# Kernel tuning notes

Hardware: AMD Instinct MI355X
Metric: run time of the kernel (lower is better)

The kernel has to match this reference:

```python
import jax, jax.numpy as jnp
import numpy as np

N = 2048          # num_nodes
F = 32            # out_features
B = 8             # batch size
DEG = 32          # avg degree for random adjacency


def _make_edge_mask(key):
    # adjacency with density DEG/N, diagonal forced to 1, plus leading ones column
    p = DEG / N
    adj = jax.random.bernoulli(key, p, (N, N))
    adj = adj | jnp.eye(N, dtype=bool)
    adj = jnp.concatenate([jnp.ones((N, 1), dtype=bool), adj], axis=1)  # [N, N+1]
    return ~adj  # True => masked (zeroed), matching mask = 1 - adj


def setup_inputs() -> dict:
    key = jax.random.key(0)
    k1, k2, k3, k4 = jax.random.split(key, 4)
    x = jax.random.normal(k1, (B, N + 1, N), dtype=jnp.float32)
    weight = jax.random.normal(k2, (N, N + 1, F), dtype=jnp.float32) * (1.0 / np.sqrt(N + 1))
    bias = jax.random.normal(k3, (F, N), dtype=jnp.float32) * 0.02
    edge_mask = _make_edge_mask(k4)  # [N, N+1] bool, True = zero
    return {"x": x, "weight": weight, "bias": bias, "edge_mask": edge_mask}


def reference(x, weight, bias, edge_mask):
    # x: [B, N+1, N] -> per-node rows [B, N, N+1]
    xt = jnp.transpose(x, (0, 2, 1))                       # [B, N, N+1]
    xm = jnp.where(edge_mask[None, :, :], 0.0, xt)          # masked_fill_
    # per-node matmul against its own weight slab [N+1, F]
    ans = jnp.einsum('bnk,nkf->bnf', xm, weight)            # [B, N, F]
    ans = jnp.transpose(ans, (0, 2, 1))                     # [B, F, N]
    return ans + bias[None, :, :]
```

## Files before the change

kernel.cpp:

```cpp
#include <hip/hip_runtime.h>


constexpr int N_ = 2048;
constexpr int K_ = 2049;
constexpr int F_ = 32;
constexpr int B_ = 8;
constexpr int CH = 9;
constexpr int CAPK = 192;

__global__ __launch_bounds__(256, 8) void snl_sparse2(
    const float* __restrict__ x,
    const float* __restrict__ w,
    const float* __restrict__ bias,
    const int*   __restrict__ em,
    float* __restrict__ out)
{
    const int bid = blockIdx.x;
    const int n   = ((bid & 7) << 8) | (bid >> 3);
    const int t   = threadIdx.x;
    const int lane   = t & 63;
    const int wid    = t >> 6;
    const int kphase = t >> 5;
    const int f      = t & 31;

    __shared__ int   s_cnt[CH * 4];
    __shared__ int   s_idx[CAPK];
    __shared__ float s_x[CAPK][B_];
    __shared__ float s_red[8][B_][F_];

    const int*   emn = em + (size_t)n * K_;
    const float* wn  = w  + (size_t)n * K_ * F_;

    int emr[CH];
    #pragma unroll
    for (int c = 0; c < CH - 1; ++c) emr[c] = emn[c * 256 + t];
    emr[CH - 1] = (t == 0) ? emn[2048] : 1;

    const unsigned long long lowmask = (1ull << lane) - 1ull;
    int woff[CH];
    unsigned actmask = 0;
    #pragma unroll
    for (int c = 0; c < CH; ++c) {
        const unsigned long long bal = __ballot(emr[c] == 0);
        if (lane == 0) s_cnt[c * 4 + wid] = __popcll(bal);
        woff[c] = __popcll(bal & lowmask);
        actmask |= (emr[c] == 0 ? 1u : 0u) << c;
    }
    __syncthreads();

    int ct = 0;
    #pragma unroll
    for (int c = 0; c < CH; ++c) {
        const int c0 = s_cnt[c * 4 + 0];
        const int c1 = s_cnt[c * 4 + 1];
        const int c2 = s_cnt[c * 4 + 2];
        const int c3 = s_cnt[c * 4 + 3];
        const int base = ct + ((wid > 0) ? c0 : 0) + ((wid > 1) ? c1 : 0) + ((wid > 2) ? c2 : 0);
        ct += c0 + c1 + c2 + c3;
        if ((actmask >> c) & 1u) {
            const int pos = base + woff[c];
            const int k   = c * 256 + t;
            if (pos < CAPK) {
                s_idx[pos] = k;
                const float* xp = x + (size_t)k * N_ + n;
                const float xv0 = xp[0 * (size_t)K_ * N_];
                const float xv1 = xp[1 * (size_t)K_ * N_];
                const float xv2 = xp[2 * (size_t)K_ * N_];
                const float xv3 = xp[3 * (size_t)K_ * N_];
                const float xv4 = xp[4 * (size_t)K_ * N_];
                const float xv5 = xp[5 * (size_t)K_ * N_];
                const float xv6 = xp[6 * (size_t)K_ * N_];
                const float xv7 = xp[7 * (size_t)K_ * N_];
                *reinterpret_cast<float4*>(&s_x[pos][0]) = make_float4(xv0, xv1, xv2, xv3);
                *reinterpret_cast<float4*>(&s_x[pos][4]) = make_float4(xv4, xv5, xv6, xv7);
            }
        }
    }

    const int ctc = (ct < CAPK) ? ct : CAPK;
    const int ctp = (ctc + 7) & ~7;
    if (t < ctp - ctc) {
        s_idx[ctc + t] = 0;
        *reinterpret_cast<float4*>(&s_x[ctc + t][0]) = make_float4(0.f, 0.f, 0.f, 0.f);
        *reinterpret_cast<float4*>(&s_x[ctc + t][4]) = make_float4(0.f, 0.f, 0.f, 0.f);
    }
    __syncthreads();

    const int tc = ctp >> 3;
    float acc[B_];
    #pragma unroll
    for (int b = 0; b < B_; ++b) acc[b] = 0.f;

    float wr[8];
    #pragma unroll
    for (int i = 0; i < 8; ++i) {
        if (i < tc) {
            const int j = kphase + i * 8;
            wr[i] = wn[(size_t)s_idx[j] * F_ + f];
        }
    }
    #pragma unroll
    for (int i = 0; i < 8; ++i) {
        if (i < tc) {
            const int j = kphase + i * 8;
            const float4 x0 = *reinterpret_cast<const float4*>(&s_x[j][0]);
            const float4 x1 = *reinterpret_cast<const float4*>(&s_x[j][4]);
            const float wv = wr[i];
            acc[0] = fmaf(x0.x, wv, acc[0]);
            acc[1] = fmaf(x0.y, wv, acc[1]);
            acc[2] = fmaf(x0.z, wv, acc[2]);
            acc[3] = fmaf(x0.w, wv, acc[3]);
            acc[4] = fmaf(x1.x, wv, acc[4]);
            acc[5] = fmaf(x1.y, wv, acc[5]);
            acc[6] = fmaf(x1.z, wv, acc[6]);
            acc[7] = fmaf(x1.w, wv, acc[7]);
        }
    }
    for (int j = kphase + 64; j < ctp; j += 8) {
        const float wv = wn[(size_t)s_idx[j] * F_ + f];
        const float4 x0 = *reinterpret_cast<const float4*>(&s_x[j][0]);
        const float4 x1 = *reinterpret_cast<const float4*>(&s_x[j][4]);
        acc[0] = fmaf(x0.x, wv, acc[0]);
        acc[1] = fmaf(x0.y, wv, acc[1]);
        acc[2] = fmaf(x0.z, wv, acc[2]);
        acc[3] = fmaf(x0.w, wv, acc[3]);
        acc[4] = fmaf(x1.x, wv, acc[4]);
        acc[5] = fmaf(x1.y, wv, acc[5]);
        acc[6] = fmaf(x1.z, wv, acc[6]);
        acc[7] = fmaf(x1.w, wv, acc[7]);
    }

    #pragma unroll
    for (int b = 0; b < B_; ++b) s_red[kphase][b][f] = acc[b];
    __syncthreads();

    {
        const int b  = t >> 5;
        const int ff = t & 31;
        float s = 0.f;
        #pragma unroll
        for (int p = 0; p < 8; ++p) s += s_red[p][b][ff];
        out[((size_t)b * F_ + ff) * N_ + n] = s + bias[(size_t)ff * N_ + n];
    }
}

extern "C" void kernel_launch(void* const* d_in, const int* in_sizes, int n_in,
                              void* d_out, int out_size, void* d_ws, size_t ws_size,
                              hipStream_t stream) {
    const float* x    = (const float*)d_in[0];
    const float* w    = (const float*)d_in[1];
    const float* bias = (const float*)d_in[2];
    const int*   em   = (const int*)d_in[3];
    float*       out  = (float*)d_out;

    snl_sparse2<<<dim3(N_), dim3(256), 0, stream>>>(x, w, bias, em, out);
}
```

Before: 21.04 us.

## Compact active indices per wavefront to drop block-wide barriers

Each wavefront now compacts its own active k indices into a private shared-memory list, so the block-wide prefix sum and two __syncthreads are no longer needed before the compute phase. The x gather is restructured so that 8 lanes load the 8 batch values of a slot in parallel, instead of one thread issuing 8 strided loads. Each wave then accumulates only its own slots with two k-phases, and the existing 8-way shared reduction combines the partial sums. A per-wave cap of 48 entries could drop nonzeros if one wave's 576 columns have more than 48 active entries, and load balance across waves depends on how the nonzeros are spread.

```diff
diff --git a/kernel.cpp b/kernel.cpp
--- a/kernel.cpp
+++ b/kernel.cpp
@@ -6,26 +6,23 @@
 constexpr int F_ = 32;
 constexpr int B_ = 8;
 constexpr int CH = 9;
-constexpr int CAPK = 192;
+constexpr int WCAP = 48;
 
-__global__ __launch_bounds__(256, 8) void snl_sparse2(
+__global__ __launch_bounds__(256, 8) void snl_sparse3(
     const float* __restrict__ x,
     const float* __restrict__ w,
     const float* __restrict__ bias,
     const int*   __restrict__ em,
     float* __restrict__ out)
 {
-    const int bid = blockIdx.x;
-    const int n   = ((bid & 7) << 8) | (bid >> 3);
-    const int t   = threadIdx.x;
-    const int lane   = t & 63;
-    const int wid    = t >> 6;
-    const int kphase = t >> 5;
-    const int f      = t & 31;
+    const int bid  = blockIdx.x;
+    const int n    = ((bid & 7) << 8) | (bid >> 3);
+    const int t    = threadIdx.x;
+    const int lane = t & 63;
+    const int wid  = t >> 6;
 
-    __shared__ int   s_cnt[CH * 4];
-    __shared__ int   s_idx[CAPK];
-    __shared__ float s_x[CAPK][B_];
+    __shared__ int   s_idx[4][WCAP];
+    __shared__ float s_x[4][WCAP][B_];
     __shared__ float s_red[8][B_][F_];
 
     const int*   emn = em + (size_t)n * K_;
@@ -37,74 +34,63 @@
     emr[CH - 1] = (t == 0) ? emn[2048] : 1;
 
     const unsigned long long lowmask = (1ull << lane) - 1ull;
-    int woff[CH];
-    unsigned actmask = 0;
+    int wcnt = 0;
     #pragma unroll
     for (int c = 0; c < CH; ++c) {
-        const unsigned long long bal = __ballot(emr[c] == 0);
-        if (lane == 0) s_cnt[c * 4 + wid] = __popcll(bal);
-        woff[c] = __popcll(bal & lowmask);
-        actmask |= (emr[c] == 0 ? 1u : 0u) << c;
+        const bool act = (emr[c] == 0);
+        const unsigned long long bal = __ballot(act);
+        const int pos = wcnt + __popcll(bal & lowmask);
+        wcnt += __popcll(bal);
+        if (act && pos < WCAP) s_idx[wid][pos] = c * 256 + t;
     }
-    __syncthreads();
+    wcnt = (wcnt < WCAP) ? wcnt : WCAP;
+    const int wcnt_p = (wcnt + 1) & ~1;
+    if (lane == 0 && (wcnt & 1)) s_idx[wid][wcnt] = 0;
 
-    int ct = 0;
-    #pragma unroll
-    for (int c = 0; c < CH; ++c) {
-        const int c0 = s_cnt[c * 4 + 0];
-        const int c1 = s_cnt[c * 4 + 1];
-        const int c2 = s_cnt[c * 4 + 2];
-        const int c3 = s_cnt[c * 4 + 3];
-        const int base = ct + ((wid > 0) ? c0 : 0) + ((wid > 1) ? c1 : 0) + ((wid > 2) ? c2 : 0);
-        ct += c0 + c1 + c2 + c3;
-        if ((actmask >> c) & 1u) {
-            const int pos = base + woff[c];
-            const int k   = c * 256 + t;
-            if (pos < CAPK) {
-                s_idx[pos] = k;
-                const float* xp = x + (size_t)k * N_ + n;
-                const float xv0 = xp[0 * (size_t)K_ * N_];
-                const float xv1 = xp[1 * (size_t)K_ * N_];
-                const float xv2 = xp[2 * (size_t)K_ * N_];
-                const float xv3 = xp[3 * (size_t)K_ * N_];
-                const float xv4 = xp[4 * (size_t)K_ * N_];
-                const float xv5 = xp[5 * (size_t)K_ * N_];
-                const float xv6 = xp[6 * (size_t)K_ * N_];
-                const float xv7 = xp[7 * (size_t)K_ * N_];
-                *reinterpret_cast<float4*>(&s_x[pos][0]) = make_float4(xv0, xv1, xv2, xv3);
-                *reinterpret_cast<float4*>(&s_x[pos][4]) = make_float4(xv4, xv5, xv6, xv7);
+    {
+        const int slot0 = lane >> 3;
+        const int gb    = lane & 7;
+        #pragma unroll
+        for (int r = 0; r < 2; ++r) {
+            const int slot = slot0 + r * 8;
+            if (slot < wcnt_p) {
+                float xv = 0.f;
+                if (slot < wcnt) {
+                    const int kj = s_idx[wid][slot];
+                    xv = x[((size_t)gb * K_ + kj) * N_ + n];
+                }
+                s_x[wid][slot][gb] = xv;
             }
+        }
+        for (int slot = slot0 + 16; slot < wcnt_p; slot += 8) {
+            float xv = 0.f;
+            if (slot < wcnt) xv = x[((size_t)gb * K_ + s_idx[wid][slot]) * N_ + n];
+            s_x[wid][slot][gb] = xv;
         }
     }
 
-    const int ctc = (ct < CAPK) ? ct : CAPK;
-    const int ctp = (ctc + 7) & ~7;
-    if (t < ctp - ctc) {
-        s_idx[ctc + t] = 0;
-        *reinterpret_cast<float4*>(&s_x[ctc + t][0]) = make_float4(0.f, 0.f, 0.f, 0.f);
-        *reinterpret_cast<float4*>(&s_x[ctc + t][4]) = make_float4(0.f, 0.f, 0.f, 0.f);
+    const int kp2 = lane >> 5;
+    const int f   = lane & 31;
+    const int tc  = wcnt_p >> 1;
+    float wr[8];
+    #pragma unroll
+    for (int i = 0; i < 8; ++i) {
+        if (i < tc) {
+            const int slot = kp2 + 2 * i;
+            wr[i] = wn[(size_t)s_idx[wid][slot] * F_ + f];
+        }
     }
-    __syncthreads();
 
-    const int tc = ctp >> 3;
     float acc[B_];
     #pragma unroll
     for (int b = 0; b < B_; ++b) acc[b] = 0.f;
 
-    float wr[8];
     #pragma unroll
     for (int i = 0; i < 8; ++i) {
         if (i < tc) {
-            const int j = kphase + i * 8;
-            wr[i] = wn[(size_t)s_idx[j] * F_ + f];
-        }
-    }
-    #pragma unroll
-    for (int i = 0; i < 8; ++i) {
-        if (i < tc) {
-            const int j = kphase + i * 8;
-            const float4 x0 = *reinterpret_cast<const float4*>(&s_x[j][0]);
-            const float4 x1 = *reinterpret_cast<const float4*>(&s_x[j][4]);
+            const int slot = kp2 + 2 * i;
+            const float4 x0 = *reinterpret_cast<const float4*>(&s_x[wid][slot][0]);
+            const float4 x1 = *reinterpret_cast<const float4*>(&s_x[wid][slot][4]);
             const float wv = wr[i];
             acc[0] = fmaf(x0.x, wv, acc[0]);
             acc[1] = fmaf(x0.y, wv, acc[1]);
@@ -116,10 +102,10 @@
             acc[7] = fmaf(x1.w, wv, acc[7]);
         }
     }
-    for (int j = kphase + 64; j < ctp; j += 8) {
-        const float wv = wn[(size_t)s_idx[j] * F_ + f];
-        const float4 x0 = *reinterpret_cast<const float4*>(&s_x[j][0]);
-        const float4 x1 = *reinterpret_cast<const float4*>(&s_x[j][4]);
+    for (int slot = kp2 + 16; slot < wcnt_p; slot += 2) {
+        const float wv = wn[(size_t)s_idx[wid][slot] * F_ + f];
+        const float4 x0 = *reinterpret_cast<const float4*>(&s_x[wid][slot][0]);
+        const float4 x1 = *reinterpret_cast<const float4*>(&s_x[wid][slot][4]);
         acc[0] = fmaf(x0.x, wv, acc[0]);
         acc[1] = fmaf(x0.y, wv, acc[1]);
         acc[2] = fmaf(x0.z, wv, acc[2]);
@@ -131,7 +117,7 @@
     }
 
     #pragma unroll
-    for (int b = 0; b < B_; ++b) s_red[kphase][b][f] = acc[b];
+    for (int b = 0; b < B_; ++b) s_red[wid * 2 + kp2][b][f] = acc[b];
     __syncthreads();
 
     {
@@ -153,5 +139,5 @@
     const int*   em   = (const int*)d_in[3];
     float*       out  = (float*)d_out;
 
-    snl_sparse2<<<dim3(N_), dim3(256), 0, stream>>>(x, w, bias, em, out);
+    snl_sparse3<<<dim3(N_), dim3(256), 0, stream>>>(x, w, bias, em, out);
 }
```

Result: no change. 20.84 us (-0.9%).
